# Optimization experiments

Hardware: AMD Instinct MI355X
Metric: run time of the kernel (lower is better)

The kernel has to match this reference:

```python
import jax, jax.numpy as jnp
import numpy as np
from jax import lax

EPS = 1e-5
N_WIRES, N_LAYERS = 4, 3
DIM = 2 ** N_WIRES  # 16

# Static CNOT permutations for control w, target w+1 (state @ CNOT => new[k] = old[k ^ (((k>>c)&1)<<t)])
_idx = np.arange(DIM)
CNOT_PERMS = [jnp.asarray(_idx ^ (((_idx >> w) & 1) << (w + 1))) for w in range(N_WIRES - 1)]


def conv3x3(x, w):
    # x: [B,1,H,W], w: [1,1,3,3], padding=1, no bias
    return lax.conv_general_dilated(x, w, (1, 1), 'SAME',
                                    dimension_numbers=('NCHW', 'OIHW', 'NCHW'))


def batchnorm_train(x, gamma, beta):
    # training-mode BN: batch statistics over (B,H,W), biased variance
    mean = jnp.mean(x, axis=(0, 2, 3), keepdims=True)
    var = jnp.var(x, axis=(0, 2, 3), keepdims=True)
    xn = (x - mean) * lax.rsqrt(var + EPS)
    return xn * gamma.reshape(1, -1, 1, 1) + beta.reshape(1, -1, 1, 1)


def residual_block(x, w1, g1, b1, w2, g2, b2):
    out = jax.nn.relu(batchnorm_train(conv3x3(x, w1), g1, b1))
    out = batchnorm_train(conv3x3(out, w2), g2, b2)
    return jax.nn.relu(out + x)


def quantum_feat4(theta):
    # Faithful to QuantumKernel: real state, each RZ scales by cos(theta/2)
    # (rz[0,0]==rz[1,1]==cos(theta/2)), CNOT is a bit-indexed permutation.
    # State is independent of the patch values (patch is never used).
    s = jnp.zeros(DIM, dtype=theta.dtype).at[0].set(1.0)
    for l in range(N_LAYERS):
        s = s * jnp.prod(jnp.cos(theta[l] / 2.0))  # 8 RZ scalings for this layer
        for w in range(N_WIRES - 1):
            s = s[CNOT_PERMS[w]]
    probs = s ** 2
    return probs[:4]


def setup_inputs() -> dict:
    key = jax.random.key(0)
    ks = jax.random.split(key, 12)
    B = 16384
    d = dict(
        x=jax.random.normal(ks[0], (B, 1, 28, 28), dtype=jnp.float32),
        theta=jax.random.normal(ks[1], (N_LAYERS, N_WIRES, 2), dtype=jnp.float32),
        r1_w1=jax.random.normal(ks[2], (1, 1, 3, 3), dtype=jnp.float32) * 0.3,
        r1_g1=jnp.ones((1,), jnp.float32), r1_b1=jnp.zeros((1,), jnp.float32),
        r1_w2=jax.random.normal(ks[3], (1, 1, 3, 3), dtype=jnp.float32) * 0.3,
        r1_g2=jnp.ones((1,), jnp.float32), r1_b2=jnp.zeros((1,), jnp.float32),
        r2_w1=jax.random.normal(ks[4], (1, 1, 3, 3), dtype=jnp.float32) * 0.3,
        r2_g1=jnp.ones((1,), jnp.float32), r2_b1=jnp.zeros((1,), jnp.float32),
        r2_w2=jax.random.normal(ks[5], (1, 1, 3, 3), dtype=jnp.float32) * 0.3,
        r2_g2=jnp.ones((1,), jnp.float32), r2_b2=jnp.zeros((1,), jnp.float32),
        fc_w=jax.random.normal(ks[6], (10, 784), dtype=jnp.float32) * 0.03,
        fc_b=jnp.zeros((10,), jnp.float32),
        alpha=jnp.asarray(0.5, dtype=jnp.float32),
    )
    return d


def reference(x, theta, r1_w1, r1_g1, r1_b1, r1_w2, r1_g2, r1_b2,
              r2_w1, r2_g1, r2_b1, r2_w2, r2_g2, r2_b2, fc_w, fc_b, alpha):
    B = x.shape[0]
    cls_feat = residual_block(x, r1_w1, r1_g1, r1_b1, r1_w2, r1_g2, r1_b2)
    cls_feat = residual_block(cls_feat, r2_w1, r2_g1, r2_b1, r2_w2, r2_g2, r2_b2)
    cls_flat = cls_feat.reshape(B, -1)  # [B, 784]

    # Quantum filter: kernel output ignores patch values, identical for all
    # 196 patches and all batch elements; cat along dim=1 -> tile the 4-vector.
    p4 = quantum_feat4(theta)                           # [4]
    q_feat = jnp.broadcast_to(jnp.tile(p4, 14 * 14), (B, 784))

    fused = alpha * cls_flat + (1.0 - alpha) * q_feat
    logits = fused @ fc_w.T + fc_b
    return jax.nn.log_softmax(logits, axis=-1)
```

## Files before the change

### kernel.cpp

```cpp
#include <hip/hip_runtime.h>
#include <hip/hip_fp16.h>
#include <math.h>

#define BATCH   16384
#define IMGPIX  784
#define NTOT    (BATCH * IMGPIX)
#define NSLOT   64
#define SLOTSTR 8
#define STAGE_DBL (NSLOT * SLOTSTR)

struct __align__(8) h4 { __half2 lo, hi; };
__device__ __forceinline__ h4 f4_to_h4(float4 v) {
    h4 r; r.lo = __floats2half2_rn(v.x, v.y); r.hi = __floats2half2_rn(v.z, v.w); return r;
}
__device__ __forceinline__ float4 h4_to_f4(h4 p) {
    float2 a = __half22float2(p.lo), b = __half22float2(p.hi);
    return make_float4(a.x, a.y, b.x, b.y);
}

__device__ __forceinline__ void wave_stats_atomic(double lsum, double lsq, double* slot) {
    #pragma unroll
    for (int off = 32; off >= 1; off >>= 1) {
        lsum += __shfl_down(lsum, off, 64);
        lsq  += __shfl_down(lsq,  off, 64);
    }
    if ((threadIdx.x & 63) == 0) {
        atomicAdd(&slot[0], lsum);
        atomicAdd(&slot[1], lsq);
    }
}

__device__ __forceinline__ float2 stats_ab(const double* __restrict__ stats_in,
                                           float gamma, float beta) {
    int lane = threadIdx.x & 63;
    double s = stats_in[lane * SLOTSTR];
    double q = stats_in[lane * SLOTSTR + 1];
    #pragma unroll
    for (int off = 32; off >= 1; off >>= 1) {
        s += __shfl_down(s, off, 64);
        q += __shfl_down(q, off, 64);
    }
    s = __shfl(s, 0, 64);
    q = __shfl(q, 0, 64);
    const double INV_N = 1.0 / (double)NTOT;
    double mean = s * INV_N;
    double var  = q * INV_N - mean * mean;
    float rstd = 1.0f / sqrtf((float)var + 1e-5f);
    float a  = gamma * rstd;
    float bb = beta - (float)mean * a;
    return make_float2(a, bb);
}


__device__ __forceinline__ float4 hrow(float wl, float wc, float wr,
                                       float L, float4 v, float R) {
    float4 h;
    h.x = fmaf(wl, L,   fmaf(wc, v.x, wr * v.y));
    h.y = fmaf(wl, v.x, fmaf(wc, v.y, wr * v.z));
    h.z = fmaf(wl, v.y, fmaf(wc, v.z, wr * v.w));
    h.w = fmaf(wl, v.z, fmaf(wc, v.w, wr * R));
    return h;
}

__device__ __forceinline__ void emit_row(__half* dst, int r, float4 o, float mf,
                                         double& lsum, double& lsq, bool act) {
    if (act) *(h4*)(dst + r * 28) = f4_to_h4(o);
    float s4 = (o.x + o.y) + (o.z + o.w);
    float q4 = fmaf(o.x, o.x, fmaf(o.y, o.y, fmaf(o.z, o.z, o.w * o.w)));
    lsum += (double)(mf * s4);
    lsq  += (double)(mf * q4);
}

#define LANE_SETUP()                                                          \
    const int t = threadIdx.x;                                                \
    const int lane = t & 63;                                                  \
    const int widx = t >> 6;                                                  \
    const int c4   = lane & 7;                                                \
    const bool act = (c4 < 7);                                                \
    const float mf = act ? 1.f : 0.f;                                         \
    const int c4c  = c4 < 7 ? c4 : 6;          \
    const int g    = blockIdx.x & 511;                       \
    const int s    = blockIdx.x >> 9;                         \
    const int r0   = s * 7;                                                   \
    const int rtop = (r0 > 0)  ? (r0 - 1) : 0;         \
    const int rbot = (r0 < 21) ? (r0 + 7) : 27;                               \
    const int img  = g * 32 + widx * 8 + (lane >> 3);                         \
    const size_t ibase = (size_t)img * IMGPIX + c4c * 4;

#define CONV_STEP(k, v)                                                       \
    {                                                                         \
        float L = __shfl_up((v).w, 1, 64);  if (c4 == 0) L = 0.f;             \
        float R = __shfl_down((v).x, 1, 64); if (c4 == 6) R = 0.f;            \
        float4 h2 = hrow(w9[6], w9[7], w9[8], L, (v), R);                     \
        float4 h1 = hrow(w9[3], w9[4], w9[5], L, (v), R);                     \
        float4 h0 = hrow(w9[0], w9[1], w9[2], L, (v), R);                     \
        accA.x += h2.x; accA.y += h2.y; accA.z += h2.z; accA.w += h2.w;       \
        if ((k) >= 2) emit_row(dst, r0 + (k) - 2, accA, mf, lsum, lsq, act);  \
        accA.x = accB.x + h1.x; accA.y = accB.y + h1.y;                       \
        accA.z = accB.z + h1.z; accA.w = accB.w + h1.w;                       \
        accB = h0;                                                            \
    }

#define HALO_ZERO(k, v)                                                       \
    if ((k) == 0 && r0 == 0)  (v) = ZERO4;                                    \
    if ((k) == 8 && r0 == 21) (v) = ZERO4;

#define ZERO4 make_float4(0.f, 0.f, 0.f, 0.f)

__global__ __launch_bounds__(256, 5) void k_conv_plain(const float* __restrict__ in,
        const float* __restrict__ w, __half* __restrict__ out, double* __restrict__ stats_out)
{
    LANE_SETUP();
    float w9[9];
    #pragma unroll
    for (int i = 0; i < 9; i++) w9[i] = w[i];
    const float* src = in + ibase;
    __half* dst = out + (size_t)img * IMGPIX + c4 * 4;

    float4 vb[9];
    vb[0] = *(const float4*)(src + rtop * 28);
    #pragma unroll
    for (int k = 1; k < 8; k++) vb[k] = *(const float4*)(src + (r0 - 1 + k) * 28);
    vb[8] = *(const float4*)(src + rbot * 28);
    __builtin_amdgcn_sched_barrier(0);

    float4 accA = ZERO4, accB = ZERO4;
    double lsum = 0.0, lsq = 0.0;
    #pragma unroll
    for (int k = 0; k < 9; k++) {
        float4 v = vb[k];
        HALO_ZERO(k, v);
        CONV_STEP(k, v);
    }
    wave_stats_atomic(lsum, lsq, &stats_out[((blockIdx.x * 4 + widx) & (NSLOT - 1)) * SLOTSTR]);
}

__global__ __launch_bounds__(256, 8) void k_conv_affine(const __half* __restrict__ in,
        const double* __restrict__ stats_in,
        const float* __restrict__ gamma, const float* __restrict__ beta,
        const float* __restrict__ w, __half* __restrict__ out, double* __restrict__ stats_out)
{
    LANE_SETUP();
    float2 ab = stats_ab(stats_in, gamma[0], beta[0]);
    float w9[9];
    #pragma unroll
    for (int i = 0; i < 9; i++) w9[i] = w[i];
    const __half* src = in + ibase;
    __half* dst = out + (size_t)img * IMGPIX + c4 * 4;

    h4 vb[9];
    vb[0] = *(const h4*)(src + rtop * 28);
    #pragma unroll
    for (int k = 1; k < 8; k++) vb[k] = *(const h4*)(src + (r0 - 1 + k) * 28);
    vb[8] = *(const h4*)(src + rbot * 28);
    __builtin_amdgcn_sched_barrier(0);

    float4 accA = ZERO4, accB = ZERO4;
    double lsum = 0.0, lsq = 0.0;
    #pragma unroll
    for (int k = 0; k < 9; k++) {
        float4 r4 = h4_to_f4(vb[k]);
        float4 v;
        v.x = fmaxf(fmaf(ab.x, r4.x, ab.y), 0.f);
        v.y = fmaxf(fmaf(ab.x, r4.y, ab.y), 0.f);
        v.z = fmaxf(fmaf(ab.x, r4.z, ab.y), 0.f);
        v.w = fmaxf(fmaf(ab.x, r4.w, ab.y), 0.f);
        HALO_ZERO(k, v);
        CONV_STEP(k, v);
    }
    wave_stats_atomic(lsum, lsq, &stats_out[((blockIdx.x * 4 + widx) & (NSLOT - 1)) * SLOTSTR]);
}

__global__ __launch_bounds__(256, 5) void k_conv_resid(const __half* __restrict__ y2,
        const float* __restrict__ x, const double* __restrict__ stats_in,
        const float* __restrict__ gamma, const float* __restrict__ beta,
        const float* __restrict__ w, __half* __restrict__ y3_out,
        __half* __restrict__ o1_out, double* __restrict__ stats_out)
{
    LANE_SETUP();
    float2 ab = stats_ab(stats_in, gamma[0], beta[0]);
    float w9[9];
    #pragma unroll
    for (int i = 0; i < 9; i++) w9[i] = w[i];
    const __half* srcy = y2 + ibase;
    const float*  srcx = x + ibase;
    __half* dst  = y3_out + (size_t)img * IMGPIX + c4 * 4;
    __half* dsto = o1_out + (size_t)img * IMGPIX + c4 * 4;

    h4 yb[9];
    float4 xb[9];
    yb[0] = *(const h4*)(srcy + rtop * 28);
    xb[0] = *(const float4*)(srcx + rtop * 28);
    #pragma unroll
    for (int k = 1; k < 8; k++) {
        yb[k] = *(const h4*)(srcy + (r0 - 1 + k) * 28);
        xb[k] = *(const float4*)(srcx + (r0 - 1 + k) * 28);
    }
    yb[8] = *(const h4*)(srcy + rbot * 28);
    xb[8] = *(const float4*)(srcx + rbot * 28);
    __builtin_amdgcn_sched_barrier(0);

    float4 accA = ZERO4, accB = ZERO4;
    double lsum = 0.0, lsq = 0.0;
    #pragma unroll
    for (int k = 0; k < 9; k++) {
        float4 r4 = h4_to_f4(yb[k]);
        float4 x4 = xb[k];
        float4 v;
        v.x = fmaxf(fmaf(ab.x, r4.x, ab.y) + x4.x, 0.f);
        v.y = fmaxf(fmaf(ab.x, r4.y, ab.y) + x4.y, 0.f);
        v.z = fmaxf(fmaf(ab.x, r4.z, ab.y) + x4.z, 0.f);
        v.w = fmaxf(fmaf(ab.x, r4.w, ab.y) + x4.w, 0.f);
        HALO_ZERO(k, v);
        if (act && k >= 1 && k <= 7)
            *(h4*)(dsto + (r0 - 1 + k) * 28) = f4_to_h4(v);
        CONV_STEP(k, v);
    }
    wave_stats_atomic(lsum, lsq, &stats_out[((blockIdx.x * 4 + widx) & (NSLOT - 1)) * SLOTSTR]);
}

#define FC_LD 11
__global__ __launch_bounds__(256) void k_head(const __half* __restrict__ y4,
        const __half* __restrict__ o1, const double* __restrict__ stats_in,
        const float* __restrict__ gamma, const float* __restrict__ beta,
        const float* __restrict__ fc_w, const float* __restrict__ qk,
        const float* __restrict__ alpha_p, float* __restrict__ out)
{
    __shared__ float fcT[IMGPIX * FC_LD];
    const int t = threadIdx.x;
    float2 ab = stats_ab(stats_in, gamma[0], beta[0]);
    for (int i = t; i < 7840; i += 256) {
        int k = i / 784;
        int j = i - k * 784;
        fcT[j * FC_LD + k] = fc_w[i];
    }
    float alpha = alpha_p[0];
    float qkr[10];
    #pragma unroll
    for (int k = 0; k < 10; k++) qkr[k] = qk[k];
    __syncthreads();

    const int wid  = t >> 6;
    const int lane = t & 63;
    const int rbase = blockIdx.x * 16 + wid * 4;

    #pragma unroll
    for (int rp = 0; rp < 2; rp++) {
        const int r0 = rbase + rp * 2;
        const __half* ya = y4 + (size_t)r0 * IMGPIX;
        const __half* yb = ya + IMGPIX;
        const __half* oa = o1 + (size_t)r0 * IMGPIX;
        const __half* ob = oa + IMGPIX;

        float acc0[10], acc1[10];
        #pragma unroll
        for (int k = 0; k < 10; k++) { acc0[k] = 0.f; acc1[k] = 0.f; }

        #pragma unroll
        for (int it = 0; it < 13; it++) {
            int j  = lane + it * 64;
            int jc = j < IMGPIX ? j : IMGPIX - 1;
            float msk = j < IMGPIX ? 1.f : 0.f;
            float va = fmaxf(fmaf(ab.x, __half2float(ya[jc]), ab.y) + __half2float(oa[jc]), 0.f) * msk;
            float vb = fmaxf(fmaf(ab.x, __half2float(yb[jc]), ab.y) + __half2float(ob[jc]), 0.f) * msk;
            const float* fr = &fcT[jc * FC_LD];
            #pragma unroll
            for (int k = 0; k < 10; k++) {
                float f = fr[k];
                acc0[k] = fmaf(va, f, acc0[k]);
                acc1[k] = fmaf(vb, f, acc1[k]);
            }
        }
        #pragma unroll
        for (int k = 0; k < 10; k++) {
            #pragma unroll
            for (int off = 1; off < 64; off <<= 1) {
                acc0[k] += __shfl_xor(acc0[k], off, 64);
                acc1[k] += __shfl_xor(acc1[k], off, 64);
            }
        }
        float l0[10], l1[10];
        float m0 = -1e30f, m1 = -1e30f;
        #pragma unroll
        for (int k = 0; k < 10; k++) {
            l0[k] = fmaf(alpha, acc0[k], qkr[k]);
            l1[k] = fmaf(alpha, acc1[k], qkr[k]);
            m0 = fmaxf(m0, l0[k]);
            m1 = fmaxf(m1, l1[k]);
        }
        float se0 = 0.f, se1 = 0.f;
        #pragma unroll
        for (int k = 0; k < 10; k++) {
            se0 += __expf(l0[k] - m0);
            se1 += __expf(l1[k] - m1);
        }
        float lse0 = m0 + __logf(se0);
        float lse1 = m1 + __logf(se1);
        if (lane < 10) {
            out[(size_t)r0 * 10 + lane]       = l0[lane] - lse0;
            out[(size_t)(r0 + 1) * 10 + lane] = l1[lane] - lse1;
        }
    }
}

__global__ __launch_bounds__(256) void k_init(const float* __restrict__ theta,
        const float* __restrict__ fc_w, const float* __restrict__ fc_b,
        const float* __restrict__ alpha_p, float* __restrict__ qk, double* __restrict__ stats)
{
    const int t = threadIdx.x;
    for (int i = t; i < 4 * STAGE_DBL; i += 256) stats[i] = 0.0;
    if (t < 10) {
        float c = 1.f;
        #pragma unroll
        for (int i = 0; i < 24; i++) c *= cosf(theta[i] * 0.5f);
        float c2 = c * c;
        float s = 0.f;
        for (int j = 0; j < 784; j += 4) s += fc_w[t * 784 + j];
        qk[t] = (1.f - alpha_p[0]) * c2 * s + fc_b[t];
    }
}

extern "C" void kernel_launch(void* const* d_in, const int* in_sizes, int n_in,
                              void* d_out, int out_size, void* d_ws, size_t ws_size,
                              hipStream_t stream) {
    const float* x     = (const float*)d_in[0];
    const float* theta = (const float*)d_in[1];
    const float* r1_w1 = (const float*)d_in[2];
    const float* r1_g1 = (const float*)d_in[3];
    const float* r1_b1 = (const float*)d_in[4];
    const float* r1_w2 = (const float*)d_in[5];
    const float* r1_g2 = (const float*)d_in[6];
    const float* r1_b2 = (const float*)d_in[7];
    const float* r2_w1 = (const float*)d_in[8];
    const float* r2_g1 = (const float*)d_in[9];
    const float* r2_b1 = (const float*)d_in[10];
    const float* r2_w2 = (const float*)d_in[11];
    const float* r2_g2 = (const float*)d_in[12];
    const float* r2_b2 = (const float*)d_in[13];
    const float* fc_w  = (const float*)d_in[14];
    const float* fc_b  = (const float*)d_in[15];
    const float* alpha = (const float*)d_in[16];
    float* out = (float*)d_out;

    double* stats = (double*)d_ws;
    float*  qk    = (float*)((char*)d_ws + 16384);
    __half* bufA  = (__half*)((char*)d_ws + 32768);
    __half* bufB  = bufA + (size_t)NTOT;
    __half* bufD  = bufB + (size_t)NTOT;

    double* s_y1 = stats + 0 * STAGE_DBL;
    double* s_y2 = stats + 1 * STAGE_DBL;
    double* s_y3 = stats + 2 * STAGE_DBL;
    double* s_y4 = stats + 3 * STAGE_DBL;

    k_init<<<1, 256, 0, stream>>>(theta, fc_w, fc_b, alpha, qk, stats);
    k_conv_plain<<<2048, 256, 0, stream>>>(x, r1_w1, bufA, s_y1);
    k_conv_affine<<<2048, 256, 0, stream>>>(bufA, s_y1, r1_g1, r1_b1, r1_w2, bufB, s_y2);
    k_conv_resid<<<2048, 256, 0, stream>>>(bufB, x, s_y2, r1_g2, r1_b2, r2_w1, bufA, bufD, s_y3);
    k_conv_affine<<<2048, 256, 0, stream>>>(bufA, s_y3, r2_g1, r2_b1, r2_w2, bufB, s_y4);
    k_head<<<1024, 256, 0, stream>>>(bufB, bufD, s_y4, r2_g2, r2_b2, fc_w, qk, alpha, out);
}
```

Before: 110.4 us.

## Interleave fp16 intermediates across 8-image groups and restructure head kernel

Intermediate half buffers move from per-image row-major to a layout where the 8 images of a wave share each 224-element row, so each wave's 8-byte stores and loads form contiguous segments instead of 8 separate strided ones. The head kernel is rewritten to match: each lane reads h4 vectors along rows, dots them against fc weights kept in original [10,784] order in LDS with float4 reads, and reduces over only 8 lanes. This drops the 13-iteration scalar loop and the 64-lane shuffle reduction. The head grid is halved and occupancy bounds are raised on two conv kernels, which may increase register pressure.

```diff
diff --git a/kernel.cpp b/kernel.cpp
--- a/kernel.cpp
+++ b/kernel.cpp
@@ -8,6 +8,8 @@
 #define NSLOT   64
 #define SLOTSTR 8
 #define STAGE_DBL (NSLOT * SLOTSTR)
+#define TROW 224
+#define TGRP 6272
 
 struct __align__(8) h4 { __half2 lo, hi; };
 __device__ __forceinline__ h4 f4_to_h4(float4 v) {
@@ -51,7 +53,6 @@
     return make_float2(a, bb);
 }
 
-
 __device__ __forceinline__ float4 hrow(float wl, float wc, float wr,
                                        float L, float4 v, float R) {
     float4 h;
@@ -64,7 +65,7 @@
 
 __device__ __forceinline__ void emit_row(__half* dst, int r, float4 o, float mf,
                                          double& lsum, double& lsq, bool act) {
-    if (act) *(h4*)(dst + r * 28) = f4_to_h4(o);
+    if (act) *(h4*)(dst + r * TROW) = f4_to_h4(o);
     float s4 = (o.x + o.y) + (o.z + o.w);
     float q4 = fmaf(o.x, o.x, fmaf(o.y, o.y, fmaf(o.z, o.z, o.w * o.w)));
     lsum += (double)(mf * s4);
@@ -79,13 +80,17 @@
     const bool act = (c4 < 7);                                                \
     const float mf = act ? 1.f : 0.f;                                         \
     const int c4c  = c4 < 7 ? c4 : 6;          \
-    const int g    = blockIdx.x & 511;                       \
+    const int g    = blockIdx.x & 511;                 \
     const int s    = blockIdx.x >> 9;                         \
     const int r0   = s * 7;                                                   \
     const int rtop = (r0 > 0)  ? (r0 - 1) : 0;         \
     const int rbot = (r0 < 21) ? (r0 + 7) : 27;                               \
-    const int img  = g * 32 + widx * 8 + (lane >> 3);                         \
-    const size_t ibase = (size_t)img * IMGPIX + c4c * 4;
+    const int i8   = lane >> 3;                                               \
+    const int G    = g * 4 + widx;                 \
+    const int img  = G * 8 + i8;                                              \
+    const size_t xbase = (size_t)img * IMGPIX + c4c * 4;           \
+    const size_t tbR   = (size_t)G * TGRP + c4c * 32 + i8 * 4;     \
+    const size_t tbW   = (size_t)G * TGRP + c4  * 32 + i8 * 4;
 
 #define CONV_STEP(k, v)                                                       \
     {                                                                         \
@@ -107,15 +112,15 @@
 
 #define ZERO4 make_float4(0.f, 0.f, 0.f, 0.f)
 
-__global__ __launch_bounds__(256, 5) void k_conv_plain(const float* __restrict__ in,
+__global__ __launch_bounds__(256, 8) void k_conv_plain(const float* __restrict__ in,
         const float* __restrict__ w, __half* __restrict__ out, double* __restrict__ stats_out)
 {
     LANE_SETUP();
     float w9[9];
     #pragma unroll
     for (int i = 0; i < 9; i++) w9[i] = w[i];
-    const float* src = in + ibase;
-    __half* dst = out + (size_t)img * IMGPIX + c4 * 4;
+    const float* src = in + xbase;
+    __half* dst = out + tbW;
 
     float4 vb[9];
     vb[0] = *(const float4*)(src + rtop * 28);
@@ -145,14 +150,14 @@
     float w9[9];
     #pragma unroll
     for (int i = 0; i < 9; i++) w9[i] = w[i];
-    const __half* src = in + ibase;
-    __half* dst = out + (size_t)img * IMGPIX + c4 * 4;
+    const __half* src = in + tbR;
+    __half* dst = out + tbW;
 
     h4 vb[9];
-    vb[0] = *(const h4*)(src + rtop * 28);
-    #pragma unroll
-    for (int k = 1; k < 8; k++) vb[k] = *(const h4*)(src + (r0 - 1 + k) * 28);
-    vb[8] = *(const h4*)(src + rbot * 28);
+    vb[0] = *(const h4*)(src + rtop * TROW);
+    #pragma unroll
+    for (int k = 1; k < 8; k++) vb[k] = *(const h4*)(src + (r0 - 1 + k) * TROW);
+    vb[8] = *(const h4*)(src + rbot * TROW);
     __builtin_amdgcn_sched_barrier(0);
 
     float4 accA = ZERO4, accB = ZERO4;
@@ -171,7 +176,7 @@
     wave_stats_atomic(lsum, lsq, &stats_out[((blockIdx.x * 4 + widx) & (NSLOT - 1)) * SLOTSTR]);
 }
 
-__global__ __launch_bounds__(256, 5) void k_conv_resid(const __half* __restrict__ y2,
+__global__ __launch_bounds__(256, 6) void k_conv_resid(const __half* __restrict__ y2,
         const float* __restrict__ x, const double* __restrict__ stats_in,
         const float* __restrict__ gamma, const float* __restrict__ beta,
         const float* __restrict__ w, __half* __restrict__ y3_out,
@@ -182,21 +187,21 @@
     float w9[9];
     #pragma unroll
     for (int i = 0; i < 9; i++) w9[i] = w[i];
-    const __half* srcy = y2 + ibase;
-    const float*  srcx = x + ibase;
-    __half* dst  = y3_out + (size_t)img * IMGPIX + c4 * 4;
-    __half* dsto = o1_out + (size_t)img * IMGPIX + c4 * 4;
+    const __half* srcy = y2 + tbR;
+    const float*  srcx = x + xbase;
+    __half* dst  = y3_out + tbW;
+    __half* dsto = o1_out + tbW;
 
     h4 yb[9];
     float4 xb[9];
-    yb[0] = *(const h4*)(srcy + rtop * 28);
+    yb[0] = *(const h4*)(srcy + rtop * TROW);
     xb[0] = *(const float4*)(srcx + rtop * 28);
     #pragma unroll
     for (int k = 1; k < 8; k++) {
-        yb[k] = *(const h4*)(srcy + (r0 - 1 + k) * 28);
+        yb[k] = *(const h4*)(srcy + (r0 - 1 + k) * TROW);
         xb[k] = *(const float4*)(srcx + (r0 - 1 + k) * 28);
     }
-    yb[8] = *(const h4*)(srcy + rbot * 28);
+    yb[8] = *(const h4*)(srcy + rbot * TROW);
     xb[8] = *(const float4*)(srcx + rbot * 28);
     __builtin_amdgcn_sched_barrier(0);
 
@@ -213,93 +218,81 @@
         v.w = fmaxf(fmaf(ab.x, r4.w, ab.y) + x4.w, 0.f);
         HALO_ZERO(k, v);
         if (act && k >= 1 && k <= 7)
-            *(h4*)(dsto + (r0 - 1 + k) * 28) = f4_to_h4(v);
+            *(h4*)(dsto + (r0 - 1 + k) * TROW) = f4_to_h4(v);
         CONV_STEP(k, v);
     }
     wave_stats_atomic(lsum, lsq, &stats_out[((blockIdx.x * 4 + widx) & (NSLOT - 1)) * SLOTSTR]);
 }
 
-#define FC_LD 11
 __global__ __launch_bounds__(256) void k_head(const __half* __restrict__ y4,
         const __half* __restrict__ o1, const double* __restrict__ stats_in,
         const float* __restrict__ gamma, const float* __restrict__ beta,
         const float* __restrict__ fc_w, const float* __restrict__ qk,
         const float* __restrict__ alpha_p, float* __restrict__ out)
 {
-    __shared__ float fcT[IMGPIX * FC_LD];
+    __shared__ float fcK[7840];
     const int t = threadIdx.x;
     float2 ab = stats_ab(stats_in, gamma[0], beta[0]);
-    for (int i = t; i < 7840; i += 256) {
-        int k = i / 784;
-        int j = i - k * 784;
-        fcT[j * FC_LD + k] = fc_w[i];
-    }
+    for (int idx = t; idx < 7840; idx += 256) fcK[idx] = fc_w[idx];
     float alpha = alpha_p[0];
     float qkr[10];
     #pragma unroll
     for (int k = 0; k < 10; k++) qkr[k] = qk[k];
     __syncthreads();
 
-    const int wid  = t >> 6;
     const int lane = t & 63;
-    const int rbase = blockIdx.x * 16 + wid * 4;
-
-    #pragma unroll
-    for (int rp = 0; rp < 2; rp++) {
-        const int r0 = rbase + rp * 2;
-        const __half* ya = y4 + (size_t)r0 * IMGPIX;
-        const __half* yb = ya + IMGPIX;
-        const __half* oa = o1 + (size_t)r0 * IMGPIX;
-        const __half* ob = oa + IMGPIX;
-
-        float acc0[10], acc1[10];
-        #pragma unroll
-        for (int k = 0; k < 10; k++) { acc0[k] = 0.f; acc1[k] = 0.f; }
-
-        #pragma unroll
-        for (int it = 0; it < 13; it++) {
-            int j  = lane + it * 64;
-            int jc = j < IMGPIX ? j : IMGPIX - 1;
-            float msk = j < IMGPIX ? 1.f : 0.f;
-            float va = fmaxf(fmaf(ab.x, __half2float(ya[jc]), ab.y) + __half2float(oa[jc]), 0.f) * msk;
-            float vb = fmaxf(fmaf(ab.x, __half2float(yb[jc]), ab.y) + __half2float(ob[jc]), 0.f) * msk;
-            const float* fr = &fcT[jc * FC_LD];
-            #pragma unroll
-            for (int k = 0; k < 10; k++) {
-                float f = fr[k];
-                acc0[k] = fmaf(va, f, acc0[k]);
-                acc1[k] = fmaf(vb, f, acc1[k]);
-            }
-        }
+    const int widx = t >> 6;
+    const int c4   = lane & 7;
+    const int i8   = lane >> 3;
+    const int c4c  = c4 < 7 ? c4 : 6;
+    const float mf = (c4 < 7) ? 1.f : 0.f;
+    const int G    = blockIdx.x * 4 + widx;
+    const size_t tb = (size_t)G * TGRP + c4c * 32 + i8 * 4;
+    const __half* ya = y4 + tb;
+    const __half* oa = o1 + tb;
+
+    float acc[10];
+    #pragma unroll
+    for (int k = 0; k < 10; k++) acc[k] = 0.f;
+
+    #pragma unroll 7
+    for (int r = 0; r < 28; r++) {
+        float4 yf = h4_to_f4(*(const h4*)(ya + r * TROW));
+        float4 of = h4_to_f4(*(const h4*)(oa + r * TROW));
+        float4 v;
+        v.x = fmaxf(fmaf(ab.x, yf.x, ab.y) + of.x, 0.f);
+        v.y = fmaxf(fmaf(ab.x, yf.y, ab.y) + of.y, 0.f);
+        v.z = fmaxf(fmaf(ab.x, yf.z, ab.y) + of.z, 0.f);
+        v.w = fmaxf(fmaf(ab.x, yf.w, ab.y) + of.w, 0.f);
+        const float* fb = &fcK[r * 28 + c4c * 4];
         #pragma unroll
         for (int k = 0; k < 10; k++) {
-            #pragma unroll
-            for (int off = 1; off < 64; off <<= 1) {
-                acc0[k] += __shfl_xor(acc0[k], off, 64);
-                acc1[k] += __shfl_xor(acc1[k], off, 64);
-            }
+            const float4 f = *(const float4*)(fb + k * 784);
+            acc[k] = fmaf(v.x, f.x, fmaf(v.y, f.y, fmaf(v.z, f.z, fmaf(v.w, f.w, acc[k]))));
         }
-        float l0[10], l1[10];
-        float m0 = -1e30f, m1 = -1e30f;
+    }
+    #pragma unroll
+    for (int k = 0; k < 10; k++) {
+        acc[k] *= mf;
+        acc[k] += __shfl_xor(acc[k], 1, 64);
+        acc[k] += __shfl_xor(acc[k], 2, 64);
+        acc[k] += __shfl_xor(acc[k], 4, 64);
+    }
+    float l[10];
+    float m = -1e30f;
+    #pragma unroll
+    for (int k = 0; k < 10; k++) {
+        l[k] = fmaf(alpha, acc[k], qkr[k]);
+        m = fmaxf(m, l[k]);
+    }
+    float se = 0.f;
+    #pragma unroll
+    for (int k = 0; k < 10; k++) se += __expf(l[k] - m);
+    float lse = m + __logf(se);
+    if (c4 == 0) {
+        int img = G * 8 + i8;
         #pragma unroll
-        for (int k = 0; k < 10; k++) {
-            l0[k] = fmaf(alpha, acc0[k], qkr[k]);
-            l1[k] = fmaf(alpha, acc1[k], qkr[k]);
-            m0 = fmaxf(m0, l0[k]);
-            m1 = fmaxf(m1, l1[k]);
-        }
-        float se0 = 0.f, se1 = 0.f;
-        #pragma unroll
-        for (int k = 0; k < 10; k++) {
-            se0 += __expf(l0[k] - m0);
-            se1 += __expf(l1[k] - m1);
-        }
-        float lse0 = m0 + __logf(se0);
-        float lse1 = m1 + __logf(se1);
-        if (lane < 10) {
-            out[(size_t)r0 * 10 + lane]       = l0[lane] - lse0;
-            out[(size_t)(r0 + 1) * 10 + lane] = l1[lane] - lse1;
-        }
+        for (int k = 0; k < 10; k++) out[(size_t)img * 10 + k] = l[k] - lse;
     }
 }
 
@@ -358,5 +351,5 @@
     k_conv_affine<<<2048, 256, 0, stream>>>(bufA, s_y1, r1_g1, r1_b1, r1_w2, bufB, s_y2);
     k_conv_resid<<<2048, 256, 0, stream>>>(bufB, x, s_y2, r1_g2, r1_b2, r2_w1, bufA, bufD, s_y3);
     k_conv_affine<<<2048, 256, 0, stream>>>(bufA, s_y3, r2_g1, r2_b1, r2_w2, bufB, s_y4);
-    k_head<<<1024, 256, 0, stream>>>(bufB, bufD, s_y4, r2_g2, r2_b2, fc_w, qk, alpha, out);
-}
+    k_head<<<512, 256, 0, stream>>>(bufB, bufD, s_y4, r2_g2, r2_b2, fc_w, qk, alpha, out);
+}
```

Result: no change. 108.5 us (-1.7%).
